# Performance work log

Measured on AMD Instinct MI355X. Metric: run time of the kernel, lower is better.

The kernel has to match this reference:

```python
import jax, jax.numpy as jnp
import numpy as np

NEG_MASK = -1.0e9  # matches torch masked_fill value


def setup_inputs() -> dict:
    key = jax.random.key(0)
    k1, k2, k3 = jax.random.split(key, 3)
    B, L, H, D = 4, 2048, 16, 64
    queries = jax.random.normal(k1, (B, L, H, D), dtype=jnp.float32)
    keys = jax.random.normal(k2, (B, L, H, D), dtype=jnp.float32)
    values = jax.random.normal(k3, (B, L, H, D), dtype=jnp.float32)
    return {"queries": queries, "keys": keys, "values": values}


def reference(queries, keys, values):
    # queries/keys/values: [B, L, H, D]
    B, L_q, H, D = queries.shape
    L_k = keys.shape[1]
    scale = 1.0 / jnp.sqrt(jnp.float32(D))
    # scores: [B, H, L_q, L_k]
    scores = jnp.einsum("blhd,bshd->bhls", queries, keys)
    # causal mask: allow s <= l (tril), fill disallowed with -1e9 BEFORE scaling,
    # exactly as the torch module does (masked_fill then softmax(scale*scores)).
    causal = jnp.tril(jnp.ones((L_q, L_k), dtype=bool))  # [L_q, L_k]
    scores = jnp.where(causal[None, None, :, :], scores, NEG_MASK)
    attn = jax.nn.softmax(scale * scores, axis=-1)  # dropout p=0.0 -> identity
    out = jnp.einsum("bhls,bshd->blhd", attn, values)
    return out
```

## Files before the change

### kernel.cpp

```cpp
#include <hip/hip_runtime.h>

typedef __attribute__((ext_vector_type(8))) short bf16x8;
typedef __attribute__((ext_vector_type(8))) unsigned short u16x8;
typedef __attribute__((ext_vector_type(4))) float f32x4;
typedef __attribute__((ext_vector_type(16))) float f32x16;

#define MFMA32 __builtin_amdgcn_mfma_f32_32x32x16_bf16
#define MFMA16 __builtin_amdgcn_mfma_f32_16x16x32_bf16

constexpr int Bc = 4, Lc = 2048, Hc = 16, Dc = 64;
constexpr float SCL = 0.18033688011112042f;

__device__ __forceinline__ unsigned short f2bf(float f) {
  unsigned u = __float_as_uint(f);
  u += 0x7fff + ((u >> 16) & 1);
  return (unsigned short)(u >> 16);
}

__device__ __forceinline__ float fexp2(float x) {
  return __builtin_amdgcn_exp2f(x);
}

__device__ __forceinline__ unsigned cvtpk(float a, float b) {
  unsigned r;
  asm("v_cvt_pk_bf16_f32 %0, %1, %2" : "=v"(r) : "v"(a), "v"(b));
  return r;
}

__device__ __forceinline__ void glds16(const char* g, char* l) {
  __builtin_amdgcn_global_load_lds(
      (const __attribute__((address_space(1))) unsigned*)g,
      (__attribute__((address_space(3))) unsigned*)l, 16, 0, 0);
}

__global__ __launch_bounds__(256)
void prep6_kernel(const float* __restrict__ Kg, const float* __restrict__ Vg,
                  char* __restrict__ KB, char* __restrict__ VB) {
  __shared__ __align__(16) short vt[64 * 80];

  const int bid = blockIdx.x;
  const int bh = bid >> 5;
  const int t  = bid & 31;
  const int b  = bh >> 4;
  const int h  = bh & 15;

  const int tid = threadIdx.x;
  const int r   = tid >> 2;
  const int seg = (tid & 3) * 16;

  const size_t srow = ((size_t)((b * Lc + t * 64 + r) * Hc + h)) * Dc + seg;
  char* ktile = KB + (size_t)(bh * 32 + t) * 8192;
  char* vtile = VB + (size_t)(bh * 32 + t) * 8192;

  {
    const float* kp = Kg + srow;
    float4 c0 = *reinterpret_cast<const float4*>(kp + 0);
    float4 c1 = *reinterpret_cast<const float4*>(kp + 4);
    float4 c2 = *reinterpret_cast<const float4*>(kp + 8);
    float4 c3 = *reinterpret_cast<const float4*>(kp + 12);
    union { unsigned u[4]; u16x8 v; } w0, w1;
    w0.u[0] = cvtpk(c0.x, c0.y); w0.u[1] = cvtpk(c0.z, c0.w);
    w0.u[2] = cvtpk(c1.x, c1.y); w0.u[3] = cvtpk(c1.z, c1.w);
    w1.u[0] = cvtpk(c2.x, c2.y); w1.u[1] = cvtpk(c2.z, c2.w);
    w1.u[2] = cvtpk(c3.x, c3.y); w1.u[3] = cvtpk(c3.z, c3.w);
    const int kc   = seg >> 4;
    const int kt2  = r >> 5;
    const int lane = r & 31;
    *reinterpret_cast<u16x8*>(ktile + ((kt2 * 4 + kc) * 64 + lane) * 16) = w0.v;
    *reinterpret_cast<u16x8*>(ktile + ((kt2 * 4 + kc) * 64 + lane + 32) * 16) = w1.v;
  }

  {
    const float* vp = Vg + srow;
    float4 v0 = *reinterpret_cast<const float4*>(vp + 0);
    float4 v1 = *reinterpret_cast<const float4*>(vp + 4);
    float4 v2 = *reinterpret_cast<const float4*>(vp + 8);
    float4 v3 = *reinterpret_cast<const float4*>(vp + 12);
    float vv[16];
    vv[0] = v0.x; vv[1] = v0.y; vv[2] = v0.z; vv[3] = v0.w;
    vv[4] = v1.x; vv[5] = v1.y; vv[6] = v1.z; vv[7] = v1.w;
    vv[8] = v2.x; vv[9] = v2.y; vv[10] = v2.z; vv[11] = v2.w;
    vv[12] = v3.x; vv[13] = v3.y; vv[14] = v3.z; vv[15] = v3.w;
#pragma unroll
    for (int j = 0; j < 16; ++j)
      vt[(seg + j) * 80 + r] = (short)f2bf(vv[j]);
  }
  __syncthreads();

  {
    const int d    = tid >> 2;
    const int kseg = (tid & 3) * 16;
    u16x8 a0 = *reinterpret_cast<const u16x8*>(vt + d * 80 + kseg);
    u16x8 a1 = *reinterpret_cast<const u16x8*>(vt + d * 80 + kseg + 8);
    const int dt2  = d >> 5;
    const int kc   = kseg >> 4;
    const int lane = d & 31;
    *reinterpret_cast<u16x8*>(vtile + ((dt2 * 4 + kc) * 64 + lane) * 16) = a0;
    *reinterpret_cast<u16x8*>(vtile + ((dt2 * 4 + kc) * 64 + lane + 32) * 16) = a1;
  }
}

__global__ __launch_bounds__(512)
void fattn9_kernel(const float* __restrict__ Qg, const char* __restrict__ KB,
                   const char* __restrict__ VB, float* __restrict__ Og) {
  __shared__ __align__(128) char smem[32768];

  const int p    = blockIdx.x;
  const int head = p & 63;
  const int qt   = 7 - (p >> 6);
  const int b    = head >> 4;
  const int h    = head & 15;

  const int tid = threadIdx.x;
  const int w   = tid >> 6;
  const int l   = tid & 63;
  const int q5  = l & 31;
  const int hp  = l >> 5;

  const int qrow = qt * 256 + w * 32 + q5;
  const int qmin = qt * 256 + w * 32;
  const int qmax = qmin + 31;

  bf16x8 qf[4];
  {
    const float* qp = Qg + ((size_t)((b * Lc + qrow) * Hc + h)) * Dc;
#pragma unroll
    for (int kc = 0; kc < 4; ++kc) {
      const int d0 = kc * 16 + hp * 8;
      float4 a = *reinterpret_cast<const float4*>(qp + d0);
      float4 bb = *reinterpret_cast<const float4*>(qp + d0 + 4);
      union { unsigned u[4]; bf16x8 v; } f;
      f.u[0] = cvtpk(a.x * SCL, a.y * SCL);
      f.u[1] = cvtpk(a.z * SCL, a.w * SCL);
      f.u[2] = cvtpk(bb.x * SCL, bb.y * SCL);
      f.u[3] = cvtpk(bb.z * SCL, bb.w * SCL);
      qf[kc] = f.v;
    }
  }

  f32x16 o0, o1;
#pragma unroll
  for (int i = 0; i < 16; ++i) { o0[i] = 0.f; o1[i] = 0.f; }
  float m_run = -3.0e38f, l_run = 0.0f;

  const char* kbase = KB + ((size_t)head * 32) * 8192;
  const char* vbase = VB + ((size_t)head * 32) * 8192;
  const int to = tid * 16;
  const int wl = w * 1024;

  auto stage = [&](int bufi, int kt) {
    const char* kb = kbase + (size_t)kt * 8192;
    const char* vb = vbase + (size_t)kt * 8192;
    char* dK = smem + bufi * 16384;
    char* dV = dK + 8192;
    glds16(kb + to, dK + wl);
    glds16(vb + to, dV + wl);
  };

  const int nkt = 4 * qt + 4;
  int buf = 0;
  stage(0, 0);

  for (int kt = 0; kt < nkt; ++kt) {
    if (kt + 1 < nkt) {
      stage(buf ^ 1, kt + 1);
      asm volatile("s_waitcnt vmcnt(2)" ::: "memory");
    } else {
      asm volatile("s_waitcnt vmcnt(0)" ::: "memory");
    }
    __builtin_amdgcn_s_barrier();

    const int kv0 = kt * 64;
    if (kv0 <= qmax) {
      const char* smK = smem + buf * 16384;
      const char* smV = smK + 8192;

      f32x16 s0, s1;
#pragma unroll
      for (int i = 0; i < 16; ++i) { s0[i] = 0.f; s1[i] = 0.f; }
#pragma unroll
      for (int kc = 0; kc < 4; ++kc) {
        bf16x8 k0 = *reinterpret_cast<const bf16x8*>(smK + (0 * 4 + kc) * 1024 + l * 16);
        bf16x8 k1 = *reinterpret_cast<const bf16x8*>(smK + (1 * 4 + kc) * 1024 + l * 16);
        s0 = MFMA32(k0, qf[kc], s0, 0, 0, 0);
        s1 = MFMA32(k1, qf[kc], s1, 0, 0, 0);
      }

      float pv[32];
#pragma unroll
      for (int g = 0; g < 16; ++g) { pv[g] = s0[g]; pv[16 + g] = s1[g]; }

      if (kv0 + 63 > qmin) {
#pragma unroll
        for (int g = 0; g < 32; ++g) {
          const int k = (g & 3) + 8 * ((g >> 2) & 3) + 4 * hp + 32 * (g >> 4);
          if (kv0 + k > qrow) pv[g] = -3.0e38f;
        }
      }

      float vmax = pv[0];
#pragma unroll
      for (int g = 1; g < 32; ++g) vmax = fmaxf(vmax, pv[g]);
      vmax = fmaxf(vmax, __shfl_xor(vmax, 32));
      if (!__all(vmax <= m_run + 8.0f)) {
        const float m_new = fmaxf(m_run, vmax);
        const float alpha = fexp2(m_run - m_new);
        l_run *= alpha;
        m_run = m_new;
#pragma unroll
        for (int i = 0; i < 16; ++i) { o0[i] *= alpha; o1[i] *= alpha; }
      }

      float rsum = 0.f;
#pragma unroll
      for (int g = 0; g < 32; ++g) { pv[g] = fexp2(pv[g] - m_run); rsum += pv[g]; }
      rsum += __shfl_xor(rsum, 32);
      l_run += rsum;

      bf16x8 pf[4];
#pragma unroll
      for (int kc = 0; kc < 4; ++kc) {
        const int G = 8 * kc;
        unsigned A0 = cvtpk(pv[G + 0], pv[G + 1]);
        unsigned A1 = cvtpk(pv[G + 2], pv[G + 3]);
        unsigned B0 = cvtpk(pv[G + 4], pv[G + 5]);
        unsigned B1 = cvtpk(pv[G + 6], pv[G + 7]);
        const unsigned t0 = hp ? A0 : B0;
        const unsigned t1 = hp ? A1 : B1;
        const unsigned x0 = (unsigned)__shfl_xor((int)t0, 32);
        const unsigned x1 = (unsigned)__shfl_xor((int)t1, 32);
        union { unsigned u[4]; bf16x8 v; } f;
        f.u[0] = hp ? x0 : A0;
        f.u[1] = hp ? x1 : A1;
        f.u[2] = hp ? B0 : x0;
        f.u[3] = hp ? B1 : x1;
        pf[kc] = f.v;
      }

#pragma unroll
      for (int kc = 0; kc < 4; ++kc) {
        bf16x8 v0 = *reinterpret_cast<const bf16x8*>(smV + (0 * 4 + kc) * 1024 + l * 16);
        bf16x8 v1 = *reinterpret_cast<const bf16x8*>(smV + (1 * 4 + kc) * 1024 + l * 16);
        o0 = MFMA32(v0, pf[kc], o0, 0, 0, 0);
        o1 = MFMA32(v1, pf[kc], o1, 0, 0, 0);
      }
    }

    __syncthreads();
    buf ^= 1;
  }

  const float inv = 1.0f / l_run;
  float* op = Og + ((size_t)((b * Lc + qrow) * Hc + h)) * Dc;
#pragma unroll
  for (int rq = 0; rq < 4; ++rq) {
    float4 st0, st1;
    st0.x = o0[4 * rq + 0] * inv; st0.y = o0[4 * rq + 1] * inv;
    st0.z = o0[4 * rq + 2] * inv; st0.w = o0[4 * rq + 3] * inv;
    st1.x = o1[4 * rq + 0] * inv; st1.y = o1[4 * rq + 1] * inv;
    st1.z = o1[4 * rq + 2] * inv; st1.w = o1[4 * rq + 3] * inv;
    *reinterpret_cast<float4*>(op + 8 * rq + 4 * hp) = st0;
    *reinterpret_cast<float4*>(op + 32 + 8 * rq + 4 * hp) = st1;
  }
}

__global__ __launch_bounds__(256)
void fattn_fallback(const float* __restrict__ Qg, const float* __restrict__ Kg,
                    const float* __restrict__ Vg, float* __restrict__ Og) {
  __shared__ __align__(128) char smem[32768];
  char* smK = smem;
  char* smV = smem + 16384;

  const int bid  = blockIdx.x;
  const int head = bid >> 5;
  const int qt   = bid & 31;
  const int b    = head >> 4;
  const int h    = head & 15;
  const int q0   = qt * 64;

  const int tid = threadIdx.x;
  const int w   = tid >> 6;
  const int l   = tid & 63;
  const int lo  = l & 15;
  const int hi4 = l >> 4;

  const int qrow = q0 + w * 16 + lo;
  const float* qp = Qg + ((size_t)((b * Lc + qrow) * Hc + h)) * Dc;
  bf16x8 qf[2];
#pragma unroll
  for (int dc = 0; dc < 2; ++dc) {
    float4 a = *reinterpret_cast<const float4*>(qp + dc * 32 + hi4 * 8);
    float4 c = *reinterpret_cast<const float4*>(qp + dc * 32 + hi4 * 8 + 4);
    bf16x8 f;
    f[0] = (short)f2bf(a.x * SCL); f[1] = (short)f2bf(a.y * SCL);
    f[2] = (short)f2bf(a.z * SCL); f[3] = (short)f2bf(a.w * SCL);
    f[4] = (short)f2bf(c.x * SCL); f[5] = (short)f2bf(c.y * SCL);
    f[6] = (short)f2bf(c.z * SCL); f[7] = (short)f2bf(c.w * SCL);
    qf[dc] = f;
  }

  f32x4 o[4];
#pragma unroll
  for (int dt = 0; dt < 4; ++dt) { o[dt][0] = 0.f; o[dt][1] = 0.f; o[dt][2] = 0.f; o[dt][3] = 0.f; }
  float m_run = -3.0e38f, l_run = 0.0f;

  const int sk   = tid >> 2;
  const int sd   = (tid & 3) * 16;
  const int swzK = (sk & 7) << 4;
  const int swzA = (lo & 7) << 4;

  const int nkt = qt + 1;
  for (int kt = 0; kt < nkt; ++kt) {
    const int kv0 = kt * 64;
    __syncthreads();
    {
      const float* kpr = Kg + ((size_t)((b * Lc + kv0 + sk) * Hc + h)) * Dc + sd;
      float4 c0 = *reinterpret_cast<const float4*>(kpr + 0);
      float4 c1 = *reinterpret_cast<const float4*>(kpr + 4);
      float4 c2 = *reinterpret_cast<const float4*>(kpr + 8);
      float4 c3 = *reinterpret_cast<const float4*>(kpr + 12);
      u16x8 w0, w1;
      w0[0] = f2bf(c0.x); w0[1] = f2bf(c0.y); w0[2] = f2bf(c0.z); w0[3] = f2bf(c0.w);
      w0[4] = f2bf(c1.x); w0[5] = f2bf(c1.y); w0[6] = f2bf(c1.z); w0[7] = f2bf(c1.w);
      w1[0] = f2bf(c2.x); w1[1] = f2bf(c2.y); w1[2] = f2bf(c2.z); w1[3] = f2bf(c2.w);
      w1[4] = f2bf(c3.x); w1[5] = f2bf(c3.y); w1[6] = f2bf(c3.z); w1[7] = f2bf(c3.w);
      *reinterpret_cast<u16x8*>(smK + sk * 128 + ((sd * 2) ^ swzK)) = w0;
      *reinterpret_cast<u16x8*>(smK + sk * 128 + ((sd * 2 + 16) ^ swzK)) = w1;

      const float* vpr = Vg + ((size_t)((b * Lc + kv0 + sk) * Hc + h)) * Dc + sd;
      float4 v0 = *reinterpret_cast<const float4*>(vpr + 0);
      float4 v1 = *reinterpret_cast<const float4*>(vpr + 4);
      float4 v2 = *reinterpret_cast<const float4*>(vpr + 8);
      float4 v3 = *reinterpret_cast<const float4*>(vpr + 12);
      float vv[16];
      vv[0] = v0.x; vv[1] = v0.y; vv[2] = v0.z; vv[3] = v0.w;
      vv[4] = v1.x; vv[5] = v1.y; vv[6] = v1.z; vv[7] = v1.w;
      vv[8] = v2.x; vv[9] = v2.y; vv[10] = v2.z; vv[11] = v2.w;
      vv[12] = v3.x; vv[13] = v3.y; vv[14] = v3.z; vv[15] = v3.w;
#pragma unroll
      for (int j = 0; j < 16; ++j) {
        const int d = sd + j;
        *reinterpret_cast<unsigned short*>(smV + d * 128 + ((sk * 2) ^ ((j & 7) << 4))) = f2bf(vv[j]);
      }
    }
    __syncthreads();

    f32x4 s[4];
#pragma unroll
    for (int ks = 0; ks < 4; ++ks) {
      const int rb = (ks * 16 + lo) * 128;
      bf16x8 a0 = *reinterpret_cast<const bf16x8*>(smK + rb + ((hi4 * 16) ^ swzA));
      bf16x8 a1 = *reinterpret_cast<const bf16x8*>(smK + rb + ((64 + hi4 * 16) ^ swzA));
      f32x4 c; c[0] = 0.f; c[1] = 0.f; c[2] = 0.f; c[3] = 0.f;
      c = MFMA16(a0, qf[0], c, 0, 0, 0);
      c = MFMA16(a1, qf[1], c, 0, 0, 0);
      s[ks] = c;
    }

    const bool diag = (kt == nkt - 1);
    float vmax = -3.0e38f;
#pragma unroll
    for (int ks = 0; ks < 4; ++ks) {
#pragma unroll
      for (int i = 0; i < 4; ++i) {
        float x = s[ks][i];
        if (diag) {
          const int kg = kv0 + ks * 16 + hi4 * 4 + i;
          if (kg > qrow) x = -3.0e38f;
        }
        s[ks][i] = x;
        vmax = fmaxf(vmax, x);
      }
    }
    vmax = fmaxf(vmax, __shfl_xor(vmax, 16));
    vmax = fmaxf(vmax, __shfl_xor(vmax, 32));
    const float m_new = fmaxf(m_run, vmax);
    const float alpha = fexp2(m_run - m_new);

    float rsum = 0.f;
    unsigned pk2[4][2];
#pragma unroll
    for (int ks = 0; ks < 4; ++ks) {
      const float p0 = fexp2(s[ks][0] - m_new);
      const float p1 = fexp2(s[ks][1] - m_new);
      const float p2 = fexp2(s[ks][2] - m_new);
      const float p3 = fexp2(s[ks][3] - m_new);
      rsum += (p0 + p1) + (p2 + p3);
      pk2[ks][0] = (unsigned)f2bf(p0) | ((unsigned)f2bf(p1) << 16);
      pk2[ks][1] = (unsigned)f2bf(p2) | ((unsigned)f2bf(p3) << 16);
    }
    rsum += __shfl_xor(rsum, 16);
    rsum += __shfl_xor(rsum, 32);
    l_run = l_run * alpha + rsum;
    m_run = m_new;
#pragma unroll
    for (int dt = 0; dt < 4; ++dt) {
      o[dt][0] *= alpha; o[dt][1] *= alpha; o[dt][2] *= alpha; o[dt][3] *= alpha;
    }

    const int srcA = lo + ((l & 16) << 1);
    const int srcB = srcA + 16;
    const bool up = (l & 32) != 0;
    bf16x8 pf[2];
#pragma unroll
    for (int c2 = 0; c2 < 2; ++c2) {
      const unsigned A0x = (unsigned)__shfl((int)pk2[2 * c2][0], srcA);
      const unsigned A0y = (unsigned)__shfl((int)pk2[2 * c2][1], srcA);
      const unsigned A1x = (unsigned)__shfl((int)pk2[2 * c2][0], srcB);
      const unsigned A1y = (unsigned)__shfl((int)pk2[2 * c2][1], srcB);
      const unsigned B0x = (unsigned)__shfl((int)pk2[2 * c2 + 1][0], srcA);
      const unsigned B0y = (unsigned)__shfl((int)pk2[2 * c2 + 1][1], srcA);
      const unsigned B1x = (unsigned)__shfl((int)pk2[2 * c2 + 1][0], srcB);
      const unsigned B1y = (unsigned)__shfl((int)pk2[2 * c2 + 1][1], srcB);
      union { unsigned u[4]; bf16x8 v; } cvt;
      cvt.u[0] = up ? B0x : A0x;
      cvt.u[1] = up ? B0y : A0y;
      cvt.u[2] = up ? B1x : A1x;
      cvt.u[3] = up ? B1y : A1y;
      pf[c2] = cvt.v;
    }

#pragma unroll
    for (int dt = 0; dt < 4; ++dt) {
      const int rb = (dt * 16 + lo) * 128;
#pragma unroll
      for (int c2 = 0; c2 < 2; ++c2) {
        bf16x8 vf = *reinterpret_cast<const bf16x8*>(smV + rb + ((c2 * 64 + hi4 * 16) ^ swzA));
        o[dt] = MFMA16(vf, pf[c2], o[dt], 0, 0, 0);
      }
    }
  }

  const float inv = 1.0f / l_run;
  float* op = Og + ((size_t)((b * Lc + qrow) * Hc + h)) * Dc;
#pragma unroll
  for (int dt = 0; dt < 4; ++dt) {
    float4 st;
    st.x = o[dt][0] * inv; st.y = o[dt][1] * inv;
    st.z = o[dt][2] * inv; st.w = o[dt][3] * inv;
    *reinterpret_cast<float4*>(op + dt * 16 + hi4 * 4) = st;
  }
}

extern "C" void kernel_launch(void* const* d_in, const int* in_sizes, int n_in,
                              void* d_out, int out_size, void* d_ws, size_t ws_size,
                              hipStream_t stream) {
  const float* Qg = (const float*)d_in[0];
  const float* Kg = (const float*)d_in[1];
  const float* Vg = (const float*)d_in[2];
  float* Og = (float*)d_out;

  const size_t blob_bytes = (size_t)64 * 32 * 8192;
  if (ws_size >= 2 * blob_bytes) {
    char* KB = (char*)d_ws;
    char* VB = KB + blob_bytes;
    hipLaunchKernelGGL(prep6_kernel, dim3(2048), dim3(256), 0, stream, Kg, Vg, KB, VB);
    hipLaunchKernelGGL(fattn9_kernel, dim3(512), dim3(512), 0, stream, Qg, KB, VB, Og);
  } else {
    hipLaunchKernelGGL(fattn_fallback, dim3(2048), dim3(256), 0, stream, Qg, Kg, Vg, Og);
  }
}
```

Baseline: 83.58 us.

## Permute V key order in prep to drop P-fragment cross-lane shuffles

The V tile layout written by the prep kernel is permuted so that the key ordering matches the MFMA output layout of the S accumulator. Each lane can then pack its own exp'd P values straight into the B operand, with no xor-32 shuffles and selects per key chunk. The per-iteration row-sum shuffle is also deferred and done once at the end, on the final l_run. The risk is getting the permutation wrong, and rescaling with a per-half l_run is only valid because alpha is uniform across the two halves.

```diff
diff --git a/kernel.cpp b/kernel.cpp
--- a/kernel.cpp
+++ b/kernel.cpp
@@ -2,6 +2,7 @@
 
 typedef __attribute__((ext_vector_type(8))) short bf16x8;
 typedef __attribute__((ext_vector_type(8))) unsigned short u16x8;
+typedef __attribute__((ext_vector_type(4))) unsigned short u16x4;
 typedef __attribute__((ext_vector_type(4))) float f32x4;
 typedef __attribute__((ext_vector_type(16))) float f32x16;
 
@@ -34,8 +35,8 @@
 }
 
 __global__ __launch_bounds__(256)
-void prep6_kernel(const float* __restrict__ Kg, const float* __restrict__ Vg,
-                  char* __restrict__ KB, char* __restrict__ VB) {
+void prep11_kernel(const float* __restrict__ Kg, const float* __restrict__ Vg,
+                   char* __restrict__ KB, char* __restrict__ VB) {
   __shared__ __align__(16) short vt[64 * 80];
 
   const int bid = blockIdx.x;
@@ -90,8 +91,15 @@
   {
     const int d    = tid >> 2;
     const int kseg = (tid & 3) * 16;
-    u16x8 a0 = *reinterpret_cast<const u16x8*>(vt + d * 80 + kseg);
-    u16x8 a1 = *reinterpret_cast<const u16x8*>(vt + d * 80 + kseg + 8);
+    u16x4 p0 = *reinterpret_cast<const u16x4*>(vt + d * 80 + kseg + 0);
+    u16x4 p1 = *reinterpret_cast<const u16x4*>(vt + d * 80 + kseg + 4);
+    u16x4 p2 = *reinterpret_cast<const u16x4*>(vt + d * 80 + kseg + 8);
+    u16x4 p3 = *reinterpret_cast<const u16x4*>(vt + d * 80 + kseg + 12);
+    u16x8 a0, a1;
+    a0[0] = p0[0]; a0[1] = p0[1]; a0[2] = p0[2]; a0[3] = p0[3];
+    a0[4] = p2[0]; a0[5] = p2[1]; a0[6] = p2[2]; a0[7] = p2[3];
+    a1[0] = p1[0]; a1[1] = p1[1]; a1[2] = p1[2]; a1[3] = p1[3];
+    a1[4] = p3[0]; a1[5] = p3[1]; a1[6] = p3[2]; a1[7] = p3[3];
     const int dt2  = d >> 5;
     const int kc   = kseg >> 4;
     const int lane = d & 31;
@@ -101,8 +109,8 @@
 }
 
 __global__ __launch_bounds__(512)
-void fattn9_kernel(const float* __restrict__ Qg, const char* __restrict__ KB,
-                   const char* __restrict__ VB, float* __restrict__ Og) {
+void fattn11_kernel(const float* __restrict__ Qg, const char* __restrict__ KB,
+                    const char* __restrict__ VB, float* __restrict__ Og) {
   __shared__ __align__(128) char smem[32768];
 
   const int p    = blockIdx.x;
@@ -214,26 +222,17 @@
       float rsum = 0.f;
 #pragma unroll
       for (int g = 0; g < 32; ++g) { pv[g] = fexp2(pv[g] - m_run); rsum += pv[g]; }
-      rsum += __shfl_xor(rsum, 32);
       l_run += rsum;
 
       bf16x8 pf[4];
 #pragma unroll
       for (int kc = 0; kc < 4; ++kc) {
         const int G = 8 * kc;
-        unsigned A0 = cvtpk(pv[G + 0], pv[G + 1]);
-        unsigned A1 = cvtpk(pv[G + 2], pv[G + 3]);
-        unsigned B0 = cvtpk(pv[G + 4], pv[G + 5]);
-        unsigned B1 = cvtpk(pv[G + 6], pv[G + 7]);
-        const unsigned t0 = hp ? A0 : B0;
-        const unsigned t1 = hp ? A1 : B1;
-        const unsigned x0 = (unsigned)__shfl_xor((int)t0, 32);
-        const unsigned x1 = (unsigned)__shfl_xor((int)t1, 32);
         union { unsigned u[4]; bf16x8 v; } f;
-        f.u[0] = hp ? x0 : A0;
-        f.u[1] = hp ? x1 : A1;
-        f.u[2] = hp ? B0 : x0;
-        f.u[3] = hp ? B1 : x1;
+        f.u[0] = cvtpk(pv[G + 0], pv[G + 1]);
+        f.u[1] = cvtpk(pv[G + 2], pv[G + 3]);
+        f.u[2] = cvtpk(pv[G + 4], pv[G + 5]);
+        f.u[3] = cvtpk(pv[G + 6], pv[G + 7]);
         pf[kc] = f.v;
       }
 
@@ -250,7 +249,8 @@
     buf ^= 1;
   }
 
-  const float inv = 1.0f / l_run;
+  const float l_tot = l_run + __shfl_xor(l_run, 32);
+  const float inv = 1.0f / l_tot;
   float* op = Og + ((size_t)((b * Lc + qrow) * Hc + h)) * Dc;
 #pragma unroll
   for (int rq = 0; rq < 4; ++rq) {
@@ -454,8 +454,8 @@
   if (ws_size >= 2 * blob_bytes) {
     char* KB = (char*)d_ws;
     char* VB = KB + blob_bytes;
-    hipLaunchKernelGGL(prep6_kernel, dim3(2048), dim3(256), 0, stream, Kg, Vg, KB, VB);
-    hipLaunchKernelGGL(fattn9_kernel, dim3(512), dim3(512), 0, stream, Qg, KB, VB, Og);
+    hipLaunchKernelGGL(prep11_kernel, dim3(2048), dim3(256), 0, stream, Kg, Vg, KB, VB);
+    hipLaunchKernelGGL(fattn11_kernel, dim3(512), dim3(512), 0, stream, Qg, KB, VB, Og);
   } else {
     hipLaunchKernelGGL(fattn_fallback, dim3(2048), dim3(256), 0, stream, Qg, Kg, Vg, Og);
   }
```

Result: faster. 77.04 us (-7.8%).
